# Optimization experiments

Measured on AMD Instinct MI355X. Metric: run time of the kernel, lower is better.

Reference implementation:

```python
import jax, jax.numpy as jnp
import numpy as np

ALPHA = 0.2  # LeakyReLU negative slope


def setup_inputs() -> dict:
    key = jax.random.key(0)
    k1, k2, k3, k4 = jax.random.split(key, 4)
    N, E, F_IN, F_OUT = 100000, 1600000, 128, 32
    x = jax.random.normal(k1, (N, F_IN), dtype=jnp.float32)
    W = jax.random.normal(k2, (F_IN, F_OUT), dtype=jnp.float32) * 0.1
    a = jax.random.normal(k3, (2 * F_OUT, 1), dtype=jnp.float32) * 0.1
    edge_index = jax.random.randint(k4, (2, E), 0, N, dtype=jnp.int64)
    return {"x": x, "W": W, "a": a, "edge_index": edge_index}


def reference(x, W, a, edge_index):
    N = x.shape[0]
    F_OUT = W.shape[1]
    Wx = x @ W  # [N, F_OUT]
    src = edge_index[0]  # row indices (softmax groups)
    dst = edge_index[1]
    # e = leakyrelu([Wx_i || Wx_j] @ a); split a to avoid materializing the concat
    a_src = a[:F_OUT, 0]
    a_dst = a[F_OUT:, 0]
    e = (Wx @ a_src)[src] + (Wx @ a_dst)[dst]  # [E]
    e = jnp.where(e >= 0, e, ALPHA * e)
    # sparse softmax over rows (src)
    m = jax.ops.segment_max(e, src, num_segments=N)  # -inf for empty rows
    m = jnp.where(jnp.isinf(m), 0.0, m)
    exp_v = jnp.exp(e - m[src])
    s = jax.ops.segment_sum(exp_v, src, num_segments=N)
    s = jnp.where(s == 0, 1.0, s)
    att = exp_v / s[src]  # [E]
    # sparse matmul: h[i] = sum_j att[i,j] * Wx[j]
    h = jax.ops.segment_sum(att[:, None] * Wx[dst], src, num_segments=N)
    return jax.nn.elu(h)
```

## Files before the change

kernel.cpp:

```cpp
#include <hip/hip_runtime.h>
#include <hip/hip_bf16.h>
#include <math.h>

#define ALPHA 0.2f
#define F_IN 128
#define F_OUT 32
#define BSHIFT 9
#define BNODES 512
#define DSTBITS 17
#define CHUNK 4096
#define SLABCAP 16384

typedef __attribute__((ext_vector_type(8))) short short8;
typedef __attribute__((ext_vector_type(4))) float float4v;

__device__ __forceinline__ short f2bf(float f) {
    __hip_bfloat16 h = __float2bfloat16(f);
    return __builtin_bit_cast(short, h);
}
__device__ __forceinline__ float bf2f(unsigned short u) {
    return __uint_as_float((unsigned)u << 16);
}

__global__ __launch_bounds__(256) void k1_mfma(
    const float* __restrict__ x, const float* __restrict__ W,
    const float* __restrict__ a, unsigned short* __restrict__ Wxh,
    float* __restrict__ s1, float* __restrict__ s2, int nTiles, int N)
{
    __shared__ short Wt[32 * 136];
    for (int i = threadIdx.x; i < F_IN * F_OUT; i += 256) {
        int k = i >> 5, n = i & 31;
        Wt[n * 136 + k] = f2bf(W[i]);
    }
    __syncthreads();

    int wave = threadIdx.x >> 6;
    int lane = threadIdx.x & 63;
    int tile = blockIdx.x * 4 + wave;
    if (tile >= nTiles) return;

    int m    = lane & 15;
    int quad = lane >> 4;
    int row  = tile * 16 + m;
    int rowc = row < N ? row : N - 1;

    short8 bf[2][4];
#pragma unroll
    for (int t = 0; t < 2; ++t)
#pragma unroll
        for (int s = 0; s < 4; ++s)
            bf[t][s] = *(const short8*)&Wt[(t * 16 + m) * 136 + s * 32 + quad * 8];

    float4v acc0 = {0.f, 0.f, 0.f, 0.f};
    float4v acc1 = {0.f, 0.f, 0.f, 0.f};
    const float* xr = x + (size_t)rowc * F_IN + quad * 8;
#pragma unroll
    for (int s = 0; s < 4; ++s) {
        float4 xa = *(const float4*)(xr + s * 32);
        float4 xb = *(const float4*)(xr + s * 32 + 4);
        short8 af;
        af[0] = f2bf(xa.x); af[1] = f2bf(xa.y); af[2] = f2bf(xa.z); af[3] = f2bf(xa.w);
        af[4] = f2bf(xb.x); af[5] = f2bf(xb.y); af[6] = f2bf(xb.z); af[7] = f2bf(xb.w);
        acc0 = __builtin_amdgcn_mfma_f32_16x16x32_bf16(af, bf[0][s], acc0, 0, 0, 0);
        acc1 = __builtin_amdgcn_mfma_f32_16x16x32_bf16(af, bf[1][s], acc1, 0, 0, 0);
    }

    int rbase = tile * 16 + quad * 4;
#pragma unroll
    for (int r = 0; r < 4; ++r) {
        if (rbase + r < N) {
            Wxh[(size_t)(rbase + r) * F_OUT + m]      = (unsigned short)f2bf(acc0[r]);
            Wxh[(size_t)(rbase + r) * F_OUT + m + 16] = (unsigned short)f2bf(acc1[r]);
        }
    }

    float a1c0 = a[m], a1c1 = a[m + 16];
    float a2c0 = a[F_OUT + m], a2c1 = a[F_OUT + m + 16];
#pragma unroll
    for (int r = 0; r < 4; ++r) {
        float v1 = acc0[r] * a1c0 + acc1[r] * a1c1;
        float v2 = acc0[r] * a2c0 + acc1[r] * a2c1;
#pragma unroll
        for (int off = 8; off >= 1; off >>= 1) {
            v1 += __shfl_xor(v1, off, 16);
            v2 += __shfl_xor(v2, off, 16);
        }
        if (m == 0 && rbase + r < N) {
            s1[rbase + r] = v1;
            s2[rbase + r] = v2;
        }
    }
}

__global__ __launch_bounds__(256) void k_bucket(
    const int* __restrict__ src, const int* __restrict__ dst,
    int* __restrict__ bcur, unsigned* __restrict__ packed, int E)
{
    __shared__ int hist[256];
    __shared__ int cur[256];
    int t = threadIdx.x;
    hist[t] = 0;
    __syncthreads();
    int e0 = blockIdx.x * CHUNK;
    int sreg[CHUNK / 256], dreg[CHUNK / 256];
#pragma unroll
    for (int k = 0; k < CHUNK / 256; ++k) {
        int e = e0 + k * 256 + t;
        if (e < E) {
            sreg[k] = src[e];
            dreg[k] = dst[e];
            atomicAdd(&hist[sreg[k] >> BSHIFT], 1);
        } else sreg[k] = -1;
    }
    __syncthreads();
    if (hist[t] > 0) cur[t] = atomicAdd(&bcur[t], hist[t]);
    __syncthreads();
#pragma unroll
    for (int k = 0; k < CHUNK / 256; ++k) {
        if (sreg[k] >= 0) {
            int b = sreg[k] >> BSHIFT;
            int p = atomicAdd(&cur[b], 1);
            if (p < SLABCAP)
                packed[(size_t)b * SLABCAP + p] =
                    ((unsigned)(sreg[k] & (BNODES - 1)) << DSTBITS) | (unsigned)dreg[k];
        }
    }
}

__global__ __launch_bounds__(256) void k_finalize(
    const unsigned* __restrict__ packed, const int* __restrict__ bcnt,
    int* __restrict__ counts, int* __restrict__ row_ptr,
    int* __restrict__ dst_sorted, int N, int NBK)
{
    __shared__ int hist[BNODES];
    __shared__ int psum[256];
    __shared__ int cur[BNODES];
    int b = blockIdx.x;
    int t = threadIdx.x;

    psum[t] = (t < b) ? min(bcnt[t], SLABCAP) : 0;
    __syncthreads();
    for (int off = 128; off >= 1; off >>= 1) {
        if (t < off) psum[t] += psum[t + off];
        __syncthreads();
    }
    int e0 = psum[0];
    __syncthreads();

    int cnt = min(bcnt[b], SLABCAP);
    const unsigned* pb = packed + (size_t)b * SLABCAP;

    hist[t] = 0; hist[t + 256] = 0;
    __syncthreads();
    for (int e = t; e < cnt; e += 256)
        atomicAdd(&hist[pb[e] >> DSTBITS], 1);
    __syncthreads();
    int a0 = hist[2 * t], a1 = hist[2 * t + 1];
    psum[t] = a0 + a1;
    __syncthreads();
    for (int off = 1; off < 256; off <<= 1) {
        int v = (t >= off) ? psum[t - off] : 0;
        __syncthreads();
        psum[t] += v;
        __syncthreads();
    }
    int excl = (t > 0) ? psum[t - 1] : 0;
    int p0 = e0 + excl;
    int p1 = p0 + a0;
    cur[2 * t] = p0;
    cur[2 * t + 1] = p1;
    int n0 = b << BSHIFT;
    if (n0 + 2 * t < N)     { counts[n0 + 2 * t] = a0;     row_ptr[n0 + 2 * t] = p0; }
    if (n0 + 2 * t + 1 < N) { counts[n0 + 2 * t + 1] = a1; row_ptr[n0 + 2 * t + 1] = p1; }
    __syncthreads();
    for (int e = t; e < cnt; e += 256) {
        unsigned v = pb[e];
        int p = atomicAdd(&cur[v >> DSTBITS], 1);
        dst_sorted[p] = v & ((1u << DSTBITS) - 1);
    }
}

__global__ __launch_bounds__(256) void k_node(
    const int* __restrict__ row_ptr, const int* __restrict__ counts,
    const int* __restrict__ dst_s,
    const float* __restrict__ s1, const float* __restrict__ s2,
    const unsigned short* __restrict__ Wxh, float* __restrict__ out, int N)
{
    int g = threadIdx.x >> 5;
    int l = threadIdx.x & 31;
    int n = blockIdx.x * 8 + g;
    if (n >= N) return;

    int base = row_ptr[n];
    int deg  = counts[n];
    float s1n = s1[n];
    int es = l >> 3;
    int fl = l & 7;

    float4 acc = {0.f, 0.f, 0.f, 0.f};
    float sum = 0.f;
    for (int j0 = 0; j0 < deg; j0 += 32) {
        int j = j0 + l;
        int   d_l = 0;
        float p_l = 0.f;
        if (j < deg) {
            d_l = dst_s[base + j];
            float ev = s1n + s2[d_l];
            ev = ev >= 0.f ? ev : ALPHA * ev;
            p_l = expf(ev);
        }
        sum += p_l;
        int cnt = min(32, deg - j0);
        int nIter = (cnt + 3) >> 2;
        for (int t = 0; t < nIter; ++t) {
            int e = t * 4 + es;
            float p = __shfl(p_l, e, 32);
            int   d = __shfl(d_l, e, 32);
            ushort4 w = *(const ushort4*)&Wxh[(size_t)d * F_OUT + fl * 4];
            acc.x += p * bf2f(w.x);
            acc.y += p * bf2f(w.y);
            acc.z += p * bf2f(w.z);
            acc.w += p * bf2f(w.w);
        }
    }
#pragma unroll
    for (int off = 8; off <= 16; off <<= 1) {
        acc.x += __shfl_xor(acc.x, off, 32);
        acc.y += __shfl_xor(acc.y, off, 32);
        acc.z += __shfl_xor(acc.z, off, 32);
        acc.w += __shfl_xor(acc.w, off, 32);
    }
#pragma unroll
    for (int off = 16; off >= 1; off >>= 1)
        sum += __shfl_xor(sum, off, 32);

    if (es == 0) {
        float inv = (deg > 0) ? 1.f / sum : 0.f;
        float4 h;
        h.x = acc.x * inv; h.y = acc.y * inv; h.z = acc.z * inv; h.w = acc.w * inv;
        h.x = h.x > 0.f ? h.x : expm1f(h.x);
        h.y = h.y > 0.f ? h.y : expm1f(h.y);
        h.z = h.z > 0.f ? h.z : expm1f(h.z);
        h.w = h.w > 0.f ? h.w : expm1f(h.w);
        *(float4*)&out[(size_t)n * F_OUT + fl * 4] = h;
    }
}

extern "C" void kernel_launch(void* const* d_in, const int* in_sizes, int n_in,
                              void* d_out, int out_size, void* d_ws, size_t ws_size,
                              hipStream_t stream)
{
    const float* x = (const float*)d_in[0];
    const float* W = (const float*)d_in[1];
    const float* a = (const float*)d_in[2];
    const int*  ei = (const int*)d_in[3];

    int N = in_sizes[0] / F_IN;
    int E = in_sizes[3] / 2;
    const int* src = ei;
    const int* dst = ei + E;
    int NBK = (N + BNODES - 1) >> BSHIFT;
    int nTiles = (N + 15) / 16;

    unsigned short* Wxh = (unsigned short*)d_ws;
    float*    s1       = (float*)d_ws + (size_t)16 * N;
    float*    s2       = s1 + N;
    int*      counts   = (int*)(s2 + N);
    int*      row_ptr  = counts + N;
    int*      bcur     = row_ptr + N;
    unsigned* packed   = (unsigned*)(bcur + 256);
    int*      dst_sorted = (int*)(packed + (size_t)NBK * SLABCAP);

    float* out = (float*)d_out;
    int nEB = (E + CHUNK - 1) / CHUNK;

    hipMemsetAsync(bcur, 0, 256 * 4, stream);

    k1_mfma<<<(nTiles + 3) / 4, 256, 0, stream>>>(x, W, a, Wxh, s1, s2, nTiles, N);
    k_bucket<<<nEB, 256, 0, stream>>>(src, dst, bcur, packed, E);
    k_finalize<<<NBK, 256, 0, stream>>>(packed, bcur, counts, row_ptr, dst_sorted, N, NBK);
    k_node<<<(N + 7) / 8, 256, 0, stream>>>(row_ptr, counts, dst_sorted, s1, s2, Wxh, out, N);
}
```

Measured before the change: 179.7 us.

## Merge projection GEMM and edge bucketing into one concurrent kernel launch

The MFMA projection kernel and the edge-bucketing kernel become one launch, with block index choosing which role a block plays, so the two independent phases run at the same time on the GPU and one launch boundary is removed. The bucketing path now loads src/dst as int4 vectors with four consecutive edges per thread, instead of strided scalar loads. The combined kernel's register and shared-memory use is the union of both roles, which may lower occupancy for each.

```diff
diff --git a/kernel.cpp b/kernel.cpp
--- a/kernel.cpp
+++ b/kernel.cpp
@@ -22,107 +22,122 @@
     return __uint_as_float((unsigned)u << 16);
 }
 
-__global__ __launch_bounds__(256) void k1_mfma(
+__global__ __launch_bounds__(256) void k_phaseA(
     const float* __restrict__ x, const float* __restrict__ W,
     const float* __restrict__ a, unsigned short* __restrict__ Wxh,
-    float* __restrict__ s1, float* __restrict__ s2, int nTiles, int N)
-{
-    __shared__ short Wt[32 * 136];
-    for (int i = threadIdx.x; i < F_IN * F_OUT; i += 256) {
-        int k = i >> 5, n = i & 31;
-        Wt[n * 136 + k] = f2bf(W[i]);
-    }
-    __syncthreads();
-
-    int wave = threadIdx.x >> 6;
-    int lane = threadIdx.x & 63;
-    int tile = blockIdx.x * 4 + wave;
-    if (tile >= nTiles) return;
-
-    int m    = lane & 15;
-    int quad = lane >> 4;
-    int row  = tile * 16 + m;
-    int rowc = row < N ? row : N - 1;
-
-    short8 bf[2][4];
-#pragma unroll
-    for (int t = 0; t < 2; ++t)
-#pragma unroll
-        for (int s = 0; s < 4; ++s)
-            bf[t][s] = *(const short8*)&Wt[(t * 16 + m) * 136 + s * 32 + quad * 8];
-
-    float4v acc0 = {0.f, 0.f, 0.f, 0.f};
-    float4v acc1 = {0.f, 0.f, 0.f, 0.f};
-    const float* xr = x + (size_t)rowc * F_IN + quad * 8;
-#pragma unroll
-    for (int s = 0; s < 4; ++s) {
-        float4 xa = *(const float4*)(xr + s * 32);
-        float4 xb = *(const float4*)(xr + s * 32 + 4);
-        short8 af;
-        af[0] = f2bf(xa.x); af[1] = f2bf(xa.y); af[2] = f2bf(xa.z); af[3] = f2bf(xa.w);
-        af[4] = f2bf(xb.x); af[5] = f2bf(xb.y); af[6] = f2bf(xb.z); af[7] = f2bf(xb.w);
-        acc0 = __builtin_amdgcn_mfma_f32_16x16x32_bf16(af, bf[0][s], acc0, 0, 0, 0);
-        acc1 = __builtin_amdgcn_mfma_f32_16x16x32_bf16(af, bf[1][s], acc1, 0, 0, 0);
-    }
-
-    int rbase = tile * 16 + quad * 4;
-#pragma unroll
-    for (int r = 0; r < 4; ++r) {
-        if (rbase + r < N) {
-            Wxh[(size_t)(rbase + r) * F_OUT + m]      = (unsigned short)f2bf(acc0[r]);
-            Wxh[(size_t)(rbase + r) * F_OUT + m + 16] = (unsigned short)f2bf(acc1[r]);
-        }
-    }
-
-    float a1c0 = a[m], a1c1 = a[m + 16];
-    float a2c0 = a[F_OUT + m], a2c1 = a[F_OUT + m + 16];
-#pragma unroll
-    for (int r = 0; r < 4; ++r) {
-        float v1 = acc0[r] * a1c0 + acc1[r] * a1c1;
-        float v2 = acc0[r] * a2c0 + acc1[r] * a2c1;
-#pragma unroll
-        for (int off = 8; off >= 1; off >>= 1) {
-            v1 += __shfl_xor(v1, off, 16);
-            v2 += __shfl_xor(v2, off, 16);
-        }
-        if (m == 0 && rbase + r < N) {
-            s1[rbase + r] = v1;
-            s2[rbase + r] = v2;
-        }
-    }
-}
-
-__global__ __launch_bounds__(256) void k_bucket(
+    float* __restrict__ s1, float* __restrict__ s2, int nTiles, int N, int nT1,
     const int* __restrict__ src, const int* __restrict__ dst,
     int* __restrict__ bcur, unsigned* __restrict__ packed, int E)
 {
-    __shared__ int hist[256];
-    __shared__ int cur[256];
-    int t = threadIdx.x;
-    hist[t] = 0;
-    __syncthreads();
-    int e0 = blockIdx.x * CHUNK;
-    int sreg[CHUNK / 256], dreg[CHUNK / 256];
-#pragma unroll
-    for (int k = 0; k < CHUNK / 256; ++k) {
-        int e = e0 + k * 256 + t;
-        if (e < E) {
-            sreg[k] = src[e];
-            dreg[k] = dst[e];
-            atomicAdd(&hist[sreg[k] >> BSHIFT], 1);
-        } else sreg[k] = -1;
-    }
-    __syncthreads();
-    if (hist[t] > 0) cur[t] = atomicAdd(&bcur[t], hist[t]);
-    __syncthreads();
-#pragma unroll
-    for (int k = 0; k < CHUNK / 256; ++k) {
-        if (sreg[k] >= 0) {
-            int b = sreg[k] >> BSHIFT;
-            int p = atomicAdd(&cur[b], 1);
-            if (p < SLABCAP)
-                packed[(size_t)b * SLABCAP + p] =
-                    ((unsigned)(sreg[k] & (BNODES - 1)) << DSTBITS) | (unsigned)dreg[k];
+    if ((int)blockIdx.x < nT1) {
+        __shared__ short Wt[32 * 136];
+        for (int i = threadIdx.x; i < F_IN * F_OUT; i += 256) {
+            int k = i >> 5, n = i & 31;
+            Wt[n * 136 + k] = f2bf(W[i]);
+        }
+        __syncthreads();
+
+        int wave = threadIdx.x >> 6;
+        int lane = threadIdx.x & 63;
+        int tile = blockIdx.x * 4 + wave;
+        if (tile >= nTiles) return;
+
+        int m    = lane & 15;
+        int quad = lane >> 4;
+        int row  = tile * 16 + m;
+        int rowc = row < N ? row : N - 1;
+
+        short8 bf[2][4];
+#pragma unroll
+        for (int t = 0; t < 2; ++t)
+#pragma unroll
+            for (int s = 0; s < 4; ++s)
+                bf[t][s] = *(const short8*)&Wt[(t * 16 + m) * 136 + s * 32 + quad * 8];
+
+        float4v acc0 = {0.f, 0.f, 0.f, 0.f};
+        float4v acc1 = {0.f, 0.f, 0.f, 0.f};
+        const float* xr = x + (size_t)rowc * F_IN + quad * 8;
+#pragma unroll
+        for (int s = 0; s < 4; ++s) {
+            float4 xa = *(const float4*)(xr + s * 32);
+            float4 xb = *(const float4*)(xr + s * 32 + 4);
+            short8 af;
+            af[0] = f2bf(xa.x); af[1] = f2bf(xa.y); af[2] = f2bf(xa.z); af[3] = f2bf(xa.w);
+            af[4] = f2bf(xb.x); af[5] = f2bf(xb.y); af[6] = f2bf(xb.z); af[7] = f2bf(xb.w);
+            acc0 = __builtin_amdgcn_mfma_f32_16x16x32_bf16(af, bf[0][s], acc0, 0, 0, 0);
+            acc1 = __builtin_amdgcn_mfma_f32_16x16x32_bf16(af, bf[1][s], acc1, 0, 0, 0);
+        }
+
+        int rbase = tile * 16 + quad * 4;
+#pragma unroll
+        for (int r = 0; r < 4; ++r) {
+            if (rbase + r < N) {
+                Wxh[(size_t)(rbase + r) * F_OUT + m]      = (unsigned short)f2bf(acc0[r]);
+                Wxh[(size_t)(rbase + r) * F_OUT + m + 16] = (unsigned short)f2bf(acc1[r]);
+            }
+        }
+
+        float a1c0 = a[m], a1c1 = a[m + 16];
+        float a2c0 = a[F_OUT + m], a2c1 = a[F_OUT + m + 16];
+#pragma unroll
+        for (int r = 0; r < 4; ++r) {
+            float v1 = acc0[r] * a1c0 + acc1[r] * a1c1;
+            float v2 = acc0[r] * a2c0 + acc1[r] * a2c1;
+#pragma unroll
+            for (int off = 8; off >= 1; off >>= 1) {
+                v1 += __shfl_xor(v1, off, 16);
+                v2 += __shfl_xor(v2, off, 16);
+            }
+            if (m == 0 && rbase + r < N) {
+                s1[rbase + r] = v1;
+                s2[rbase + r] = v2;
+            }
+        }
+    } else {
+        __shared__ int hist[256];
+        __shared__ int cur[256];
+        int t = threadIdx.x;
+        hist[t] = 0;
+        __syncthreads();
+        int e0 = ((int)blockIdx.x - nT1) * CHUNK;
+        int sreg[16], dreg[16];
+#pragma unroll
+        for (int k = 0; k < 4; ++k) {
+            int e = e0 + k * 1024 + t * 4;
+            int4 s4, d4;
+            if (e + 3 < E) {
+                s4 = *(const int4*)&src[e];
+                d4 = *(const int4*)&dst[e];
+            } else {
+                s4.x = (e + 0 < E) ? src[e + 0] : -1;
+                s4.y = (e + 1 < E) ? src[e + 1] : -1;
+                s4.z = (e + 2 < E) ? src[e + 2] : -1;
+                s4.w = (e + 3 < E) ? src[e + 3] : -1;
+                d4.x = (e + 0 < E) ? dst[e + 0] : 0;
+                d4.y = (e + 1 < E) ? dst[e + 1] : 0;
+                d4.z = (e + 2 < E) ? dst[e + 2] : 0;
+                d4.w = (e + 3 < E) ? dst[e + 3] : 0;
+            }
+            sreg[k * 4 + 0] = s4.x; dreg[k * 4 + 0] = d4.x;
+            sreg[k * 4 + 1] = s4.y; dreg[k * 4 + 1] = d4.y;
+            sreg[k * 4 + 2] = s4.z; dreg[k * 4 + 2] = d4.z;
+            sreg[k * 4 + 3] = s4.w; dreg[k * 4 + 3] = d4.w;
+        }
+#pragma unroll
+        for (int k = 0; k < 16; ++k)
+            if (sreg[k] >= 0) atomicAdd(&hist[sreg[k] >> BSHIFT], 1);
+        __syncthreads();
+        if (hist[t] > 0) cur[t] = atomicAdd(&bcur[t], hist[t]);
+        __syncthreads();
+#pragma unroll
+        for (int k = 0; k < 16; ++k) {
+            if (sreg[k] >= 0) {
+                int b = sreg[k] >> BSHIFT;
+                int p = atomicAdd(&cur[b], 1);
+                if (p < SLABCAP)
+                    packed[(size_t)b * SLABCAP + p] =
+                        ((unsigned)(sreg[k] & (BNODES - 1)) << DSTBITS) | (unsigned)dreg[k];
+            }
         }
     }
 }
@@ -261,6 +276,8 @@
     const int* dst = ei + E;
     int NBK = (N + BNODES - 1) >> BSHIFT;
     int nTiles = (N + 15) / 16;
+    int nT1 = (nTiles + 3) / 4;
+    int nEB = (E + CHUNK - 1) / CHUNK;
 
     unsigned short* Wxh = (unsigned short*)d_ws;
     float*    s1       = (float*)d_ws + (size_t)16 * N;
@@ -272,12 +289,11 @@
     int*      dst_sorted = (int*)(packed + (size_t)NBK * SLABCAP);
 
     float* out = (float*)d_out;
-    int nEB = (E + CHUNK - 1) / CHUNK;
 
     hipMemsetAsync(bcur, 0, 256 * 4, stream);
 
-    k1_mfma<<<(nTiles + 3) / 4, 256, 0, stream>>>(x, W, a, Wxh, s1, s2, nTiles, N);
-    k_bucket<<<nEB, 256, 0, stream>>>(src, dst, bcur, packed, E);
+    k_phaseA<<<nT1 + nEB, 256, 0, stream>>>(x, W, a, Wxh, s1, s2, nTiles, N, nT1,
+                                            src, dst, bcur, packed, E);
     k_finalize<<<NBK, 256, 0, stream>>>(packed, bcur, counts, row_ptr, dst_sorted, N, NBK);
     k_node<<<(N + 7) / 8, 256, 0, stream>>>(row_ptr, counts, dst_sorted, s1, s2, Wxh, out, N);
 }
```

Result: faster. 170.6 us (-5.0%).
